# Kernel tuning notes

Measured on AMD Instinct MI355X. Metric: run time of the kernel, lower is better.

Reference implementation:

```python
import jax, jax.numpy as jnp
import numpy as np

N_NODES = 50000
N_EDGES = 800000
D_IN = 128
D_OUT = 128
NUM_RELS = 100


def setup_inputs() -> dict:
    key = jax.random.key(0)
    k1, k2, k3, k4, k5, k6, k7 = jax.random.split(key, 7)
    h = jax.random.normal(k1, (N_NODES, D_IN), dtype=jnp.float32)
    W = jax.random.normal(k2, (D_IN, D_OUT), dtype=jnp.float32) * 0.05
    attn = jax.random.normal(k3, (2 * D_OUT,), dtype=jnp.float32) * 0.05
    rel_emb = jax.random.normal(k4, (NUM_RELS, 1), dtype=jnp.float32)
    src = jax.random.randint(k5, (N_EDGES,), 0, N_NODES, dtype=jnp.int32)
    dst = jax.random.randint(k6, (N_EDGES,), 0, N_NODES, dtype=jnp.int32)
    etype = jax.random.randint(k7, (N_EDGES,), 0, NUM_RELS, dtype=jnp.int32)
    return {"h": h, "W": W, "attn": attn, "rel_emb": rel_emb,
            "src": src, "dst": dst, "etype": etype}


def reference(h, W, attn, rel_emb, src, dst, etype):
    # h: [N, d_in], W: [d_in, d_out], attn: [2*d_out], rel_emb: [R, 1]
    # src/dst/etype: [E]
    N = h.shape[0]
    d = W.shape[1]
    # padding_idx=0 in nn.Embedding -> row 0 is zero
    rel_table = rel_emb.at[0].set(0.0)
    z = h @ W  # [N, d_out]
    # attn_fc([z_src, z_dst]) = z_src @ a_l + z_dst @ a_r (split the concat-linear)
    s_src = z @ attn[:d]  # [N]
    s_dst = z @ attn[d:]  # [N]
    e = jax.nn.leaky_relu(s_src[src] + s_dst[dst])  # [E], slope 0.01 as in torch
    # segment softmax over incoming edges of each dst node
    m = jax.ops.segment_max(e, dst, num_segments=N)  # [N]
    ex = jnp.exp(e - m[dst])  # [E]
    denom = jax.ops.segment_sum(ex, dst, num_segments=N)  # [N]
    alpha = ex / denom[dst]  # [E]
    coef = rel_table[etype, 0] * alpha  # [E]  (rel_alpha * alpha)
    # weighted sum of source messages per destination node
    out = jax.ops.segment_sum(coef[:, None] * z[src], dst, num_segments=N)  # [N, d_out]
    return out
```

## Files before the change

kernel.cpp:

```cpp
#include <hip/hip_runtime.h>

#define D 128
#define GROWS 64

typedef __attribute__((ext_vector_type(8))) short short8;
typedef __attribute__((ext_vector_type(4))) float float4v;

__device__ __forceinline__ ushort f2bf(float x) {
    uint u = __float_as_uint(x);
    return (ushort)((u + 0x7FFFu + ((u >> 16) & 1u)) >> 16);
}
__device__ __forceinline__ float bf_lo(uint u) { return __uint_as_float(u << 16); }
__device__ __forceinline__ float bf_hi(uint u) { return __uint_as_float(u & 0xFFFF0000u); }

__global__ __launch_bounds__(256) void convW_kernel(
    const float* __restrict__ W, ushort* __restrict__ Wtg)
{
    int idx = blockIdx.x * 256 + threadIdx.x;
    int k = idx >> 7, n = idx & 127;
    Wtg[n * 128 + k] = f2bf(W[idx]);
}

__global__ __launch_bounds__(512) void gemm_mfma_kernel(
    const float* __restrict__ h, const ushort* __restrict__ Wtg,
    const float* __restrict__ attn, const int* __restrict__ dst,
    ushort* __restrict__ zb, float* __restrict__ s_src, float* __restrict__ s_dst,
    int* __restrict__ histm, int nhi, int N, int E, int nblocks)
{
    __shared__ ushort ht[GROWS * 136];
    __shared__ float psum_s[GROWS][2];
    __shared__ float psum_d[GROWS][2];
    __shared__ int histA[256];
    const int tid = threadIdx.x;
    const int base = blockIdx.x * GROWS;

#pragma unroll
    for (int it = 0; it < 4; ++it) {
        int idx = it * 512 + tid;
        int r = idx >> 5, c4 = (idx & 31) * 4;
        float4 v = make_float4(0.f, 0.f, 0.f, 0.f);
        if (base + r < N) v = *(const float4*)&h[(size_t)(base + r) * D + c4];
        ushort4 u = make_ushort4(f2bf(v.x), f2bf(v.y), f2bf(v.z), f2bf(v.w));
        *(ushort4*)&ht[r * 136 + c4] = u;
    }
    if (tid < 256) histA[tid] = 0;
    __syncthreads();

    const int lane = tid & 63;
    const int wave = tid >> 6;
    const int wr = wave >> 1;
    const int wc = wave & 1;
    const int col = lane & 15;
    const int quad = lane >> 4;
    const int wm = wr * 16;

    float4v acc[4];
#pragma unroll
    for (int nt = 0; nt < 4; ++nt) acc[nt] = (float4v)(0.f);

#pragma unroll
    for (int kc = 0; kc < 128; kc += 32) {
        short8 a = *(const short8*)&ht[(wm + col) * 136 + kc + quad * 8];
#pragma unroll
        for (int nt = 0; nt < 4; ++nt) {
            short8 b = *(const short8*)&Wtg[(wc * 64 + nt * 16 + col) * 128 + kc + quad * 8];
            acc[nt] = __builtin_amdgcn_mfma_f32_16x16x32_bf16(a, b, acc[nt], 0, 0, 0);
        }
    }
    __syncthreads();

    float ps[4] = {0.f, 0.f, 0.f, 0.f}, pd[4] = {0.f, 0.f, 0.f, 0.f};
#pragma unroll
    for (int nt = 0; nt < 4; ++nt) {
        float aL = attn[wc * 64 + nt * 16 + col];
        float aR = attn[D + wc * 64 + nt * 16 + col];
#pragma unroll
        for (int reg = 0; reg < 4; ++reg) {
            float v = acc[nt][reg];
            ps[reg] = fmaf(v, aL, ps[reg]);
            pd[reg] = fmaf(v, aR, pd[reg]);
            ht[(wm + quad * 4 + reg) * 136 + wc * 64 + nt * 16 + col] = f2bf(v);
        }
    }
#pragma unroll
    for (int reg = 0; reg < 4; ++reg) {
#pragma unroll
        for (int off = 1; off < 16; off <<= 1) {
            ps[reg] += __shfl_xor(ps[reg], off);
            pd[reg] += __shfl_xor(pd[reg], off);
        }
        if (col == 0) {
            int rl = wm + quad * 4 + reg;
            psum_s[rl][wc] = ps[reg];
            psum_d[rl][wc] = pd[reg];
        }
    }
    __syncthreads();

    if (tid < GROWS && base + tid < N) {
        s_src[base + tid] = psum_s[tid][0] + psum_s[tid][1];
        s_dst[base + tid] = psum_d[tid][0] + psum_d[tid][1];
    }

#pragma unroll
    for (int it = 0; it < 2; ++it) {
        int idx = it * 512 + tid;
        int r = idx >> 4, c8 = idx & 15;
        if (base + r < N)
            *(uint4*)&zb[(size_t)(base + r) * D + c8 * 8] = *(uint4*)&ht[r * 136 + c8 * 8];
    }

    const int cpb = (E + nblocks - 1) / nblocks;
    const int cs = blockIdx.x * cpb;
    const int ce = min(cs + cpb, E);
    for (int i = cs + tid; i < ce; i += 512)
        atomicAdd(&histA[dst[i] >> 8], 1);
    __syncthreads();
    if (tid < nhi) histm[blockIdx.x * nhi + tid] = histA[tid];
}

__global__ __launch_bounds__(64) void binB1_kernel(
    int* __restrict__ histm, int* __restrict__ colsum, int nhi, int nchunk)
{
    const int b = blockIdx.x;
    const int t = threadIdx.x;
    const int K = (nchunk + 63) / 64;
    int v[16];
    int s = 0;
#pragma unroll
    for (int j = 0; j < 16; ++j) {
        int c = t * K + j;
        v[j] = (j < K && c < nchunk) ? histm[c * nhi + b] : 0;
        s += v[j];
    }
    int incl = s;
#pragma unroll
    for (int off = 1; off < 64; off <<= 1) {
        int u = __shfl_up(incl, off);
        if (t >= off) incl += u;
    }
    int run = incl - s;
#pragma unroll
    for (int j = 0; j < 16; ++j) {
        int c = t * K + j;
        if (j < K && c < nchunk) { histm[c * nhi + b] = run; run += v[j]; }
    }
    if (t == 63) colsum[b] = incl;
}

__global__ __launch_bounds__(256) void binC_kernel(
    const int* __restrict__ src, const int* __restrict__ dst,
    const int* __restrict__ etype, const int* __restrict__ histm,
    const int* __restrict__ colsum, uint* __restrict__ binned,
    int nhi, int E, int nchunk)
{
    __shared__ int sc[256];
    __shared__ int cur[256];
    const int tid = threadIdx.x;
    int tot = (tid < nhi) ? colsum[tid] : 0;
    sc[tid] = tot;
    __syncthreads();
    for (int off = 1; off < 256; off <<= 1) {
        int u = (tid >= off) ? sc[tid - off] : 0;
        __syncthreads();
        sc[tid] += u;
        __syncthreads();
    }
    if (tid < nhi) cur[tid] = (sc[tid] - tot) + histm[blockIdx.x * nhi + tid];
    __syncthreads();
    const int cpb = (E + nchunk - 1) / nchunk;
    const int cs = blockIdx.x * cpb;
    const int ce = min(cs + cpb, E);
    for (int i = cs + tid; i < ce; i += 256) {
        int d = dst[i];
        int pos = atomicAdd(&cur[d >> 8], 1);
        binned[pos] = (uint)src[i] | ((uint)etype[i] << 16) | ((uint)(d & 255) << 23);
    }
}

__global__ __launch_bounds__(256) void binD_kernel(
    const uint* __restrict__ binned, const int* __restrict__ colsum,
    int* __restrict__ offsets, uint* __restrict__ csr, int nhi, int N, int E)
{
    __shared__ int sc[256];
    __shared__ int hist[256];
    __shared__ int cur[256];
    const int t = threadIdx.x;
    const int hi = blockIdx.x;
    int tot = (t < nhi) ? colsum[t] : 0;
    sc[t] = tot;
    __syncthreads();
    for (int off = 1; off < 256; off <<= 1) {
        int u = (t >= off) ? sc[t - off] : 0;
        __syncthreads();
        sc[t] += u;
        __syncthreads();
    }
    const int bb = (hi == 0) ? 0 : sc[hi - 1];
    const int be = sc[hi];
    hist[t] = 0;
    __syncthreads();
    for (int i = bb + t; i < be; i += 256)
        atomicAdd(&hist[(binned[i] >> 23) & 0xFF], 1);
    __syncthreads();
    int total = hist[t];
    cur[t] = total;
    __syncthreads();
    for (int off = 1; off < 256; off <<= 1) {
        int u = (t >= off) ? cur[t - off] : 0;
        __syncthreads();
        cur[t] += u;
        __syncthreads();
    }
    int excl = cur[t] - total;
    int node = hi * 256 + t;
    if (node < N) offsets[node] = bb + excl;
    if (node == N - 1) offsets[N] = E;
    __syncthreads();
    cur[t] = bb + excl;
    __syncthreads();
    for (int i = bb + t; i < be; i += 256) {
        uint pk = binned[i];
        int pos = atomicAdd(&cur[(pk >> 23) & 0xFF], 1);
        csr[pos] = pk;
    }
}

__global__ __launch_bounds__(256) void aggregate_kernel(
    const uint* __restrict__ zb32, const float* __restrict__ s_src,
    const float* __restrict__ s_dst, const int* __restrict__ offsets,
    const uint* __restrict__ csr_packed, const float* __restrict__ rel_emb,
    float* __restrict__ out, int N, int R)
{
    __shared__ float rel_l[128];
    const int tid = threadIdx.x;
    if (tid < R) rel_l[tid] = (tid == 0) ? 0.f : rel_emb[tid];
    __syncthreads();

    const int lane = tid & 63;
    const int q    = lane >> 4;
    const int ql   = lane & 15;
    const int wave = tid >> 6;
    const int d = blockIdx.x * 16 + wave * 4 + q;
    if (d >= N) return;

    const int start = offsets[d];
    const int end   = offsets[d + 1];
    const float sdst = s_dst[d];
    const int qb = q * 16;

    float m = -INFINITY, l = 0.f;
    float4 acc0 = make_float4(0.f, 0.f, 0.f, 0.f);
    float4 acc1 = make_float4(0.f, 0.f, 0.f, 0.f);

    for (int base = start; base < end; base += 16) {
        const int idx = base + ql;
        const bool valid = idx < end;
        const uint packed = valid ? csr_packed[idx] : 0;
        const int srcv = (int)(packed & 0xFFFF);
        const int et = (int)((packed >> 16) & 0x7F);
        float ev = -INFINITY;
        if (valid) {
            float x = s_src[srcv] + sdst;
            ev = (x > 0.f) ? x : 0.01f * x;
        }
        float cm = ev;
#pragma unroll
        for (int off = 8; off; off >>= 1) cm = fmaxf(cm, __shfl_xor(cm, off));
        const float newm = fmaxf(m, cm);
        const float scale = __expf(m - newm);
        const float p = valid ? __expf(ev - newm) : 0.f;
        float ssum = p;
#pragma unroll
        for (int off = 8; off; off >>= 1) ssum += __shfl_xor(ssum, off);
        l = l * scale + ssum;
        acc0.x *= scale; acc0.y *= scale; acc0.z *= scale; acc0.w *= scale;
        acc1.x *= scale; acc1.y *= scale; acc1.z *= scale; acc1.w *= scale;
        m = newm;

        const float w = p * rel_l[et];
        const int nv = min(16, end - base);
        for (int j = 0; j < nv; j += 4) {
            const float w0 = __shfl(w, qb + j);
            const float w1 = __shfl(w, qb + j + 1);
            const float w2 = __shfl(w, qb + j + 2);
            const float w3 = __shfl(w, qb + j + 3);
            const int s0 = __shfl(srcv, qb + j);
            const int s1 = __shfl(srcv, qb + j + 1);
            const int s2 = __shfl(srcv, qb + j + 2);
            const int s3 = __shfl(srcv, qb + j + 3);
            const uint4 u0 = *(const uint4*)(zb32 + (size_t)s0 * 64 + ql * 4);
            const uint4 u1 = *(const uint4*)(zb32 + (size_t)s1 * 64 + ql * 4);
            const uint4 u2 = *(const uint4*)(zb32 + (size_t)s2 * 64 + ql * 4);
            const uint4 u3 = *(const uint4*)(zb32 + (size_t)s3 * 64 + ql * 4);
            acc0.x = fmaf(w0, bf_lo(u0.x), acc0.x);
            acc0.y = fmaf(w0, bf_hi(u0.x), acc0.y);
            acc0.z = fmaf(w0, bf_lo(u0.y), acc0.z);
            acc0.w = fmaf(w0, bf_hi(u0.y), acc0.w);
            acc1.x = fmaf(w0, bf_lo(u0.z), acc1.x);
            acc1.y = fmaf(w0, bf_hi(u0.z), acc1.y);
            acc1.z = fmaf(w0, bf_lo(u0.w), acc1.z);
            acc1.w = fmaf(w0, bf_hi(u0.w), acc1.w);
            acc0.x = fmaf(w1, bf_lo(u1.x), acc0.x);
            acc0.y = fmaf(w1, bf_hi(u1.x), acc0.y);
            acc0.z = fmaf(w1, bf_lo(u1.y), acc0.z);
            acc0.w = fmaf(w1, bf_hi(u1.y), acc0.w);
            acc1.x = fmaf(w1, bf_lo(u1.z), acc1.x);
            acc1.y = fmaf(w1, bf_hi(u1.z), acc1.y);
            acc1.z = fmaf(w1, bf_lo(u1.w), acc1.z);
            acc1.w = fmaf(w1, bf_hi(u1.w), acc1.w);
            acc0.x = fmaf(w2, bf_lo(u2.x), acc0.x);
            acc0.y = fmaf(w2, bf_hi(u2.x), acc0.y);
            acc0.z = fmaf(w2, bf_lo(u2.y), acc0.z);
            acc0.w = fmaf(w2, bf_hi(u2.y), acc0.w);
            acc1.x = fmaf(w2, bf_lo(u2.z), acc1.x);
            acc1.y = fmaf(w2, bf_hi(u2.z), acc1.y);
            acc1.z = fmaf(w2, bf_lo(u2.w), acc1.z);
            acc1.w = fmaf(w2, bf_hi(u2.w), acc1.w);
            acc0.x = fmaf(w3, bf_lo(u3.x), acc0.x);
            acc0.y = fmaf(w3, bf_hi(u3.x), acc0.y);
            acc0.z = fmaf(w3, bf_lo(u3.y), acc0.z);
            acc0.w = fmaf(w3, bf_hi(u3.y), acc0.w);
            acc1.x = fmaf(w3, bf_lo(u3.z), acc1.x);
            acc1.y = fmaf(w3, bf_hi(u3.z), acc1.y);
            acc1.z = fmaf(w3, bf_lo(u3.w), acc1.z);
            acc1.w = fmaf(w3, bf_hi(u3.w), acc1.w);
        }
    }

    const float inv = (l > 0.f) ? 1.0f / l : 0.f;
    float* orow = out + (size_t)d * D + ql * 8;
    *(float4*)orow       = make_float4(acc0.x * inv, acc0.y * inv, acc0.z * inv, acc0.w * inv);
    *(float4*)(orow + 4) = make_float4(acc1.x * inv, acc1.y * inv, acc1.z * inv, acc1.w * inv);
}

extern "C" void kernel_launch(void* const* d_in, const int* in_sizes, int n_in,
                              void* d_out, int out_size, void* d_ws, size_t ws_size,
                              hipStream_t stream)
{
    const float* h    = (const float*)d_in[0];
    const float* W    = (const float*)d_in[1];
    const float* attn = (const float*)d_in[2];
    const float* rel  = (const float*)d_in[3];
    const int*   src  = (const int*)d_in[4];
    const int*   dst  = (const int*)d_in[5];
    const int*   et   = (const int*)d_in[6];
    float* out = (float*)d_out;

    const int N = in_sizes[0] / D;
    const int E = in_sizes[4];
    const int R = in_sizes[3];

    char* p = (char*)d_ws;
    auto alloc = [&](size_t bytes) {
        char* q = p;
        p += (bytes + 255) & ~(size_t)255;
        return q;
    };
    const int nhi     = (N + 255) / 256;
    const int gblocks = (N + GROWS - 1) / GROWS;

    ushort* zb     = (ushort*)alloc((size_t)N * D * sizeof(ushort));
    ushort* Wtg    = (ushort*)alloc((size_t)D * D * sizeof(ushort));
    float* ssrc    = (float*)alloc((size_t)N * sizeof(float));
    float* sdst    = (float*)alloc((size_t)N * sizeof(float));
    int*   offsets = (int*)alloc((size_t)(N + 1) * sizeof(int));
    uint*  binned  = (uint*)alloc((size_t)E * sizeof(uint));
    uint*  csr     = (uint*)alloc((size_t)E * sizeof(uint));
    int*   histm   = (int*)alloc((size_t)gblocks * nhi * sizeof(int));
    int*   colsum  = (int*)alloc((size_t)nhi * sizeof(int));

    convW_kernel<<<64, 256, 0, stream>>>(W, Wtg);
    gemm_mfma_kernel<<<gblocks, 512, 0, stream>>>(h, Wtg, attn, dst, zb, ssrc, sdst,
                                                  histm, nhi, N, E, gblocks);
    binB1_kernel<<<nhi, 64, 0, stream>>>(histm, colsum, nhi, gblocks);
    binC_kernel<<<gblocks, 256, 0, stream>>>(src, dst, et, histm, colsum, binned,
                                             nhi, E, gblocks);
    binD_kernel<<<nhi, 256, 0, stream>>>(binned, colsum, offsets, csr, nhi, N, E);
    aggregate_kernel<<<(N + 15) / 16, 256, 0, stream>>>((const uint*)zb, ssrc, sdst,
                                                        offsets, csr, rel, out, N, R);
}
```

Before: 165.7 us.

## Fuse per-bucket CSR sort into aggregation kernel using shared-memory edge lists

The second-level counting sort (binD) is merged into the aggregation kernel. Each of SPLIT blocks per 256-node bucket re-sorts the bucket's binned edges into shared memory and then aggregates its 64 nodes from that list. This removes the global CSR/offsets write and re-read and one kernel launch. In exchange, each bucket's sort is repeated SPLIT times, the grid has far fewer blocks, and each wave walks several nodes in sequence. Buckets larger than MAXBIN edges silently drop edges.

```diff
diff --git a/kernel.cpp b/kernel.cpp
--- a/kernel.cpp
+++ b/kernel.cpp
@@ -2,6 +2,8 @@
 
 #define D 128
 #define GROWS 64
+#define SPLIT 4
+#define MAXBIN 6144
 
 typedef __attribute__((ext_vector_type(8))) short short8;
 typedef __attribute__((ext_vector_type(4))) float float4v;
@@ -178,160 +180,160 @@
     }
 }
 
-__global__ __launch_bounds__(256) void binD_kernel(
-    const uint* __restrict__ binned, const int* __restrict__ colsum,
-    int* __restrict__ offsets, uint* __restrict__ csr, int nhi, int N, int E)
-{
+__global__ __launch_bounds__(256) void aggD_kernel(
+    const uint* __restrict__ zb32, const float* __restrict__ s_src,
+    const float* __restrict__ s_dst, const int* __restrict__ colsum,
+    const uint* __restrict__ binned, const float* __restrict__ rel_emb,
+    float* __restrict__ out, int nhi, int N, int R)
+{
+    __shared__ float rel_l[128];
     __shared__ int sc[256];
-    __shared__ int hist[256];
     __shared__ int cur[256];
-    const int t = threadIdx.x;
-    const int hi = blockIdx.x;
-    int tot = (t < nhi) ? colsum[t] : 0;
-    sc[t] = tot;
+    __shared__ int lo_off[257];
+    __shared__ uint sE[MAXBIN];
+    const int tid = threadIdx.x;
+    if (tid < R) rel_l[tid] = (tid == 0) ? 0.f : rel_emb[tid];
+
+    const int hi = blockIdx.x / SPLIT;
+    const int part = blockIdx.x % SPLIT;
+
+    int tot = (tid < nhi) ? colsum[tid] : 0;
+    sc[tid] = tot;
     __syncthreads();
     for (int off = 1; off < 256; off <<= 1) {
-        int u = (t >= off) ? sc[t - off] : 0;
-        __syncthreads();
-        sc[t] += u;
+        int u = (tid >= off) ? sc[tid - off] : 0;
+        __syncthreads();
+        sc[tid] += u;
         __syncthreads();
     }
     const int bb = (hi == 0) ? 0 : sc[hi - 1];
     const int be = sc[hi];
-    hist[t] = 0;
-    __syncthreads();
-    for (int i = bb + t; i < be; i += 256)
-        atomicAdd(&hist[(binned[i] >> 23) & 0xFF], 1);
-    __syncthreads();
-    int total = hist[t];
-    cur[t] = total;
+    __syncthreads();
+
+    cur[tid] = 0;
+    __syncthreads();
+    for (int i = bb + tid; i < be; i += 256)
+        atomicAdd(&cur[(binned[i] >> 23) & 0xFF], 1);
+    __syncthreads();
+    int hc = cur[tid];
+    sc[tid] = hc;
     __syncthreads();
     for (int off = 1; off < 256; off <<= 1) {
-        int u = (t >= off) ? cur[t - off] : 0;
-        __syncthreads();
-        cur[t] += u;
-        __syncthreads();
-    }
-    int excl = cur[t] - total;
-    int node = hi * 256 + t;
-    if (node < N) offsets[node] = bb + excl;
-    if (node == N - 1) offsets[N] = E;
-    __syncthreads();
-    cur[t] = bb + excl;
-    __syncthreads();
-    for (int i = bb + t; i < be; i += 256) {
+        int u = (tid >= off) ? sc[tid - off] : 0;
+        __syncthreads();
+        sc[tid] += u;
+        __syncthreads();
+    }
+    lo_off[tid + 1] = sc[tid];
+    if (tid == 0) lo_off[0] = 0;
+    cur[tid] = sc[tid] - hc;
+    __syncthreads();
+    for (int i = bb + tid; i < be; i += 256) {
         uint pk = binned[i];
         int pos = atomicAdd(&cur[(pk >> 23) & 0xFF], 1);
-        csr[pos] = pk;
-    }
-}
-
-__global__ __launch_bounds__(256) void aggregate_kernel(
-    const uint* __restrict__ zb32, const float* __restrict__ s_src,
-    const float* __restrict__ s_dst, const int* __restrict__ offsets,
-    const uint* __restrict__ csr_packed, const float* __restrict__ rel_emb,
-    float* __restrict__ out, int N, int R)
-{
-    __shared__ float rel_l[128];
-    const int tid = threadIdx.x;
-    if (tid < R) rel_l[tid] = (tid == 0) ? 0.f : rel_emb[tid];
+        if (pos < MAXBIN) sE[pos] = pk;
+    }
     __syncthreads();
 
     const int lane = tid & 63;
-    const int q    = lane >> 4;
-    const int ql   = lane & 15;
+    const int q = lane >> 4;
+    const int ql = lane & 15;
     const int wave = tid >> 6;
-    const int d = blockIdx.x * 16 + wave * 4 + q;
-    if (d >= N) return;
-
-    const int start = offsets[d];
-    const int end   = offsets[d + 1];
-    const float sdst = s_dst[d];
+    const int qid = wave * 4 + q;
     const int qb = q * 16;
 
-    float m = -INFINITY, l = 0.f;
-    float4 acc0 = make_float4(0.f, 0.f, 0.f, 0.f);
-    float4 acc1 = make_float4(0.f, 0.f, 0.f, 0.f);
-
-    for (int base = start; base < end; base += 16) {
-        const int idx = base + ql;
-        const bool valid = idx < end;
-        const uint packed = valid ? csr_packed[idx] : 0;
-        const int srcv = (int)(packed & 0xFFFF);
-        const int et = (int)((packed >> 16) & 0x7F);
-        float ev = -INFINITY;
-        if (valid) {
-            float x = s_src[srcv] + sdst;
-            ev = (x > 0.f) ? x : 0.01f * x;
-        }
-        float cm = ev;
-#pragma unroll
-        for (int off = 8; off; off >>= 1) cm = fmaxf(cm, __shfl_xor(cm, off));
-        const float newm = fmaxf(m, cm);
-        const float scale = __expf(m - newm);
-        const float p = valid ? __expf(ev - newm) : 0.f;
-        float ssum = p;
-#pragma unroll
-        for (int off = 8; off; off >>= 1) ssum += __shfl_xor(ssum, off);
-        l = l * scale + ssum;
-        acc0.x *= scale; acc0.y *= scale; acc0.z *= scale; acc0.w *= scale;
-        acc1.x *= scale; acc1.y *= scale; acc1.z *= scale; acc1.w *= scale;
-        m = newm;
-
-        const float w = p * rel_l[et];
-        const int nv = min(16, end - base);
-        for (int j = 0; j < nv; j += 4) {
-            const float w0 = __shfl(w, qb + j);
-            const float w1 = __shfl(w, qb + j + 1);
-            const float w2 = __shfl(w, qb + j + 2);
-            const float w3 = __shfl(w, qb + j + 3);
-            const int s0 = __shfl(srcv, qb + j);
-            const int s1 = __shfl(srcv, qb + j + 1);
-            const int s2 = __shfl(srcv, qb + j + 2);
-            const int s3 = __shfl(srcv, qb + j + 3);
-            const uint4 u0 = *(const uint4*)(zb32 + (size_t)s0 * 64 + ql * 4);
-            const uint4 u1 = *(const uint4*)(zb32 + (size_t)s1 * 64 + ql * 4);
-            const uint4 u2 = *(const uint4*)(zb32 + (size_t)s2 * 64 + ql * 4);
-            const uint4 u3 = *(const uint4*)(zb32 + (size_t)s3 * 64 + ql * 4);
-            acc0.x = fmaf(w0, bf_lo(u0.x), acc0.x);
-            acc0.y = fmaf(w0, bf_hi(u0.x), acc0.y);
-            acc0.z = fmaf(w0, bf_lo(u0.y), acc0.z);
-            acc0.w = fmaf(w0, bf_hi(u0.y), acc0.w);
-            acc1.x = fmaf(w0, bf_lo(u0.z), acc1.x);
-            acc1.y = fmaf(w0, bf_hi(u0.z), acc1.y);
-            acc1.z = fmaf(w0, bf_lo(u0.w), acc1.z);
-            acc1.w = fmaf(w0, bf_hi(u0.w), acc1.w);
-            acc0.x = fmaf(w1, bf_lo(u1.x), acc0.x);
-            acc0.y = fmaf(w1, bf_hi(u1.x), acc0.y);
-            acc0.z = fmaf(w1, bf_lo(u1.y), acc0.z);
-            acc0.w = fmaf(w1, bf_hi(u1.y), acc0.w);
-            acc1.x = fmaf(w1, bf_lo(u1.z), acc1.x);
-            acc1.y = fmaf(w1, bf_hi(u1.z), acc1.y);
-            acc1.z = fmaf(w1, bf_lo(u1.w), acc1.z);
-            acc1.w = fmaf(w1, bf_hi(u1.w), acc1.w);
-            acc0.x = fmaf(w2, bf_lo(u2.x), acc0.x);
-            acc0.y = fmaf(w2, bf_hi(u2.x), acc0.y);
-            acc0.z = fmaf(w2, bf_lo(u2.y), acc0.z);
-            acc0.w = fmaf(w2, bf_hi(u2.y), acc0.w);
-            acc1.x = fmaf(w2, bf_lo(u2.z), acc1.x);
-            acc1.y = fmaf(w2, bf_hi(u2.z), acc1.y);
-            acc1.z = fmaf(w2, bf_lo(u2.w), acc1.z);
-            acc1.w = fmaf(w2, bf_hi(u2.w), acc1.w);
-            acc0.x = fmaf(w3, bf_lo(u3.x), acc0.x);
-            acc0.y = fmaf(w3, bf_hi(u3.x), acc0.y);
-            acc0.z = fmaf(w3, bf_lo(u3.y), acc0.z);
-            acc0.w = fmaf(w3, bf_hi(u3.y), acc0.w);
-            acc1.x = fmaf(w3, bf_lo(u3.z), acc1.x);
-            acc1.y = fmaf(w3, bf_hi(u3.z), acc1.y);
-            acc1.z = fmaf(w3, bf_lo(u3.w), acc1.z);
-            acc1.w = fmaf(w3, bf_hi(u3.w), acc1.w);
-        }
-    }
-
-    const float inv = (l > 0.f) ? 1.0f / l : 0.f;
-    float* orow = out + (size_t)d * D + ql * 8;
-    *(float4*)orow       = make_float4(acc0.x * inv, acc0.y * inv, acc0.z * inv, acc0.w * inv);
-    *(float4*)(orow + 4) = make_float4(acc1.x * inv, acc1.y * inv, acc1.z * inv, acc1.w * inv);
+    for (int nIdx = qid; nIdx < 64; nIdx += 16) {
+        const int lo = part * 64 + nIdx;
+        const int d = hi * 256 + lo;
+        if (d >= N) continue;
+        const int st = lo_off[lo];
+        const int en = lo_off[lo + 1];
+        const float sdst = s_dst[d];
+
+        float m = -INFINITY, l = 0.f;
+        float4 acc0 = make_float4(0.f, 0.f, 0.f, 0.f);
+        float4 acc1 = make_float4(0.f, 0.f, 0.f, 0.f);
+
+        for (int b2 = st; b2 < en; b2 += 16) {
+            const int idx = b2 + ql;
+            const bool valid = idx < en;
+            const uint packed = valid ? sE[idx] : 0;
+            const int srcv = (int)(packed & 0xFFFF);
+            const int et = (int)((packed >> 16) & 0x7F);
+            float ev = -INFINITY;
+            if (valid) {
+                float x = s_src[srcv] + sdst;
+                ev = (x > 0.f) ? x : 0.01f * x;
+            }
+            float cm = ev;
+#pragma unroll
+            for (int off = 8; off; off >>= 1) cm = fmaxf(cm, __shfl_xor(cm, off));
+            const float newm = fmaxf(m, cm);
+            const float scale = __expf(m - newm);
+            const float p = valid ? __expf(ev - newm) : 0.f;
+            float ssum = p;
+#pragma unroll
+            for (int off = 8; off; off >>= 1) ssum += __shfl_xor(ssum, off);
+            l = l * scale + ssum;
+            acc0.x *= scale; acc0.y *= scale; acc0.z *= scale; acc0.w *= scale;
+            acc1.x *= scale; acc1.y *= scale; acc1.z *= scale; acc1.w *= scale;
+            m = newm;
+
+            const float w = p * rel_l[et];
+            const int nv = min(16, en - b2);
+            for (int j = 0; j < nv; j += 4) {
+                const float w0 = __shfl(w, qb + j);
+                const float w1 = __shfl(w, qb + j + 1);
+                const float w2 = __shfl(w, qb + j + 2);
+                const float w3 = __shfl(w, qb + j + 3);
+                const int s0 = __shfl(srcv, qb + j);
+                const int s1 = __shfl(srcv, qb + j + 1);
+                const int s2 = __shfl(srcv, qb + j + 2);
+                const int s3 = __shfl(srcv, qb + j + 3);
+                const uint4 u0 = *(const uint4*)(zb32 + (size_t)s0 * 64 + ql * 4);
+                const uint4 u1 = *(const uint4*)(zb32 + (size_t)s1 * 64 + ql * 4);
+                const uint4 u2 = *(const uint4*)(zb32 + (size_t)s2 * 64 + ql * 4);
+                const uint4 u3 = *(const uint4*)(zb32 + (size_t)s3 * 64 + ql * 4);
+                acc0.x = fmaf(w0, bf_lo(u0.x), acc0.x);
+                acc0.y = fmaf(w0, bf_hi(u0.x), acc0.y);
+                acc0.z = fmaf(w0, bf_lo(u0.y), acc0.z);
+                acc0.w = fmaf(w0, bf_hi(u0.y), acc0.w);
+                acc1.x = fmaf(w0, bf_lo(u0.z), acc1.x);
+                acc1.y = fmaf(w0, bf_hi(u0.z), acc1.y);
+                acc1.z = fmaf(w0, bf_lo(u0.w), acc1.z);
+                acc1.w = fmaf(w0, bf_hi(u0.w), acc1.w);
+                acc0.x = fmaf(w1, bf_lo(u1.x), acc0.x);
+                acc0.y = fmaf(w1, bf_hi(u1.x), acc0.y);
+                acc0.z = fmaf(w1, bf_lo(u1.y), acc0.z);
+                acc0.w = fmaf(w1, bf_hi(u1.y), acc0.w);
+                acc1.x = fmaf(w1, bf_lo(u1.z), acc1.x);
+                acc1.y = fmaf(w1, bf_hi(u1.z), acc1.y);
+                acc1.z = fmaf(w1, bf_lo(u1.w), acc1.z);
+                acc1.w = fmaf(w1, bf_hi(u1.w), acc1.w);
+                acc0.x = fmaf(w2, bf_lo(u2.x), acc0.x);
+                acc0.y = fmaf(w2, bf_hi(u2.x), acc0.y);
+                acc0.z = fmaf(w2, bf_lo(u2.y), acc0.z);
+                acc0.w = fmaf(w2, bf_hi(u2.y), acc0.w);
+                acc1.x = fmaf(w2, bf_lo(u2.z), acc1.x);
+                acc1.y = fmaf(w2, bf_hi(u2.z), acc1.y);
+                acc1.z = fmaf(w2, bf_lo(u2.w), acc1.z);
+                acc1.w = fmaf(w2, bf_hi(u2.w), acc1.w);
+                acc0.x = fmaf(w3, bf_lo(u3.x), acc0.x);
+                acc0.y = fmaf(w3, bf_hi(u3.x), acc0.y);
+                acc0.z = fmaf(w3, bf_lo(u3.y), acc0.z);
+                acc0.w = fmaf(w3, bf_hi(u3.y), acc0.w);
+                acc1.x = fmaf(w3, bf_lo(u3.z), acc1.x);
+                acc1.y = fmaf(w3, bf_hi(u3.z), acc1.y);
+                acc1.z = fmaf(w3, bf_lo(u3.w), acc1.z);
+                acc1.w = fmaf(w3, bf_hi(u3.w), acc1.w);
+            }
+        }
+
+        const float inv = (l > 0.f) ? 1.0f / l : 0.f;
+        float* orow = out + (size_t)d * D + ql * 8;
+        *(float4*)orow       = make_float4(acc0.x * inv, acc0.y * inv, acc0.z * inv, acc0.w * inv);
+        *(float4*)(orow + 4) = make_float4(acc1.x * inv, acc1.y * inv, acc1.z * inv, acc1.w * inv);
+    }
 }
 
 extern "C" void kernel_launch(void* const* d_in, const int* in_sizes, int n_in,
@@ -364,9 +366,7 @@
     ushort* Wtg    = (ushort*)alloc((size_t)D * D * sizeof(ushort));
     float* ssrc    = (float*)alloc((size_t)N * sizeof(float));
     float* sdst    = (float*)alloc((size_t)N * sizeof(float));
-    int*   offsets = (int*)alloc((size_t)(N + 1) * sizeof(int));
     uint*  binned  = (uint*)alloc((size_t)E * sizeof(uint));
-    uint*  csr     = (uint*)alloc((size_t)E * sizeof(uint));
     int*   histm   = (int*)alloc((size_t)gblocks * nhi * sizeof(int));
     int*   colsum  = (int*)alloc((size_t)nhi * sizeof(int));
 
@@ -376,7 +376,6 @@
     binB1_kernel<<<nhi, 64, 0, stream>>>(histm, colsum, nhi, gblocks);
     binC_kernel<<<gblocks, 256, 0, stream>>>(src, dst, et, histm, colsum, binned,
                                              nhi, E, gblocks);
-    binD_kernel<<<nhi, 256, 0, stream>>>(binned, colsum, offsets, csr, nhi, N, E);
-    aggregate_kernel<<<(N + 15) / 16, 256, 0, stream>>>((const uint*)zb, ssrc, sdst,
-                                                        offsets, csr, rel, out, N, R);
-}
+    aggD_kernel<<<nhi * SPLIT, 256, 0, stream>>>((const uint*)zb, ssrc, sdst,
+                                                 colsum, binned, rel, out, nhi, N, R);
+}
```

Measured after the change: 163.2 us. No clear change (-1.5%).
